# Optimization experiments

Hardware: AMD Instinct MI355X
Metric: run time of the kernel (lower is better)

## Reference

```python
import jax, jax.numpy as jnp
import numpy as np

D_MODEL = 1024
N_HEADS = 16
MAX_LAG = 512
D_K = D_MODEL // N_HEADS


def setup_inputs() -> dict:
    key = jax.random.key(0)
    ks = jax.random.split(key, 11)
    B, S = 2, 2048
    x = jax.random.normal(ks[0], (B, S, D_MODEL), dtype=jnp.float32)
    lag = jax.random.randint(ks[1], (S,), 0, MAX_LAG + 1, dtype=jnp.int64)
    scale = 1.0 / np.sqrt(D_MODEL)
    wq = jax.random.normal(ks[2], (D_MODEL, D_MODEL), dtype=jnp.float32) * scale
    bq = jnp.zeros((D_MODEL,), dtype=jnp.float32)
    wk = jax.random.normal(ks[3], (D_MODEL, D_MODEL), dtype=jnp.float32) * scale
    bk = jnp.zeros((D_MODEL,), dtype=jnp.float32)
    wv = jax.random.normal(ks[4], (D_MODEL, D_MODEL), dtype=jnp.float32) * scale
    bv = jnp.zeros((D_MODEL,), dtype=jnp.float32)
    wo = jax.random.normal(ks[5], (D_MODEL, D_MODEL), dtype=jnp.float32) * scale
    bo = jnp.zeros((D_MODEL,), dtype=jnp.float32)
    lag_bias = jax.random.normal(ks[6], (N_HEADS, MAX_LAG + 1), dtype=jnp.float32) * 0.02
    return {"x": x, "lag": lag, "wq": wq, "bq": bq, "wk": wk, "bk": bk,
            "wv": wv, "bv": bv, "wo": wo, "bo": bo, "lag_bias": lag_bias}


def reference(x, lag, wq, bq, wk, bk, wv, bv, wo, bo, lag_bias):
    B, S, D = x.shape
    H, dk = N_HEADS, D_K
    # projections: torch Linear is x @ W.T + b; here weights stored as (in, out)
    q = (x @ wq + bq).reshape(B, S, H, dk).transpose(0, 2, 1, 3)  # (B,H,S,dk)
    k = (x @ wk + bk).reshape(B, S, H, dk).transpose(0, 2, 1, 3)
    v = (x @ wv + bv).reshape(B, S, H, dk).transpose(0, 2, 1, 3)
    scores = jnp.einsum('bhqd,bhkd->bhqk', q, k) / jnp.sqrt(jnp.float32(dk))
    ld = jnp.abs(lag[:, None] - lag[None, :]).astype(jnp.int32)  # (S,S)
    bias = lag_bias[:, ld]  # (H,S,S)
    attn = jax.nn.softmax(scores + bias[None], axis=-1)
    out = jnp.einsum('bhqk,bhkd->bhqd', attn, v)
    out = out.transpose(0, 2, 1, 3).reshape(B, S, D)
    return out @ wo + bo
```

## Files before the change

### kernel.cpp

```cpp
#include <hip/hip_runtime.h>

typedef __bf16 bf16;
typedef __bf16 bf16x8 __attribute__((ext_vector_type(8)));
typedef float f32x4 __attribute__((ext_vector_type(4)));

__device__ __forceinline__ f32x4 mfma16(bf16x8 a, bf16x8 b, f32x4 c) {
  return __builtin_amdgcn_mfma_f32_16x16x32_bf16(a, b, c, 0, 0, 0);
}
__device__ __forceinline__ void gload16(const bf16* g, bf16* l) {
  __builtin_amdgcn_global_load_lds((const __attribute__((address_space(1))) unsigned int*)g,
                                   (__attribute__((address_space(3))) unsigned int*)l, 16, 0, 0);
}

__global__ __launch_bounds__(256) void cvt_x_kernel(const float* __restrict__ in,
                                                    bf16* __restrict__ out, int n8) {
  int i = blockIdx.x * 256 + threadIdx.x;
  if (i >= n8) return;
  const float4* p = (const float4*)in + (size_t)i * 2;
  float4 f0 = p[0], f1 = p[1];
  bf16x8 o;
  o[0] = (bf16)f0.x; o[1] = (bf16)f0.y; o[2] = (bf16)f0.z; o[3] = (bf16)f0.w;
  o[4] = (bf16)f1.x; o[5] = (bf16)f1.y; o[6] = (bf16)f1.z; o[7] = (bf16)f1.w;
  *((bf16x8*)out + i) = o;
}

__global__ __launch_bounds__(256) void cvt_wt_kernel(const float* __restrict__ in,
                                                     bf16* __restrict__ out) {
  __shared__ float t[64][68];
  int bx = blockIdx.x & 15;
  int by = blockIdx.x >> 4;
  int tid = threadIdx.x;
  int r = tid >> 2, p = tid & 3;
  const float* src = in + (size_t)(by * 64 + r) * 1024 + bx * 64 + p * 16;
#pragma unroll
  for (int j = 0; j < 16; j += 4)
    *(float4*)&t[r][p * 16 + j] = *(const float4*)(src + j);
  __syncthreads();
  int n = tid >> 2, sp = tid & 3;
  bf16 tmp[16];
#pragma unroll
  for (int j = 0; j < 16; ++j) tmp[j] = (bf16)t[sp * 16 + j][n];
  bf16* dst = out + (size_t)(bx * 64 + n) * 1024 + by * 64 + sp * 16;
  *(bf16x8*)dst = *(bf16x8*)&tmp[0];
  *(bf16x8*)(dst + 8) = *(bf16x8*)&tmp[8];
}

__global__ void cvt_bias_kernel(const float* __restrict__ bq, const float* __restrict__ bk,
                                const float* __restrict__ bv, float* __restrict__ out) {
  int i = blockIdx.x * 256 + threadIdx.x;
  if (i < 1024) out[i] = bq[i];
  else if (i < 2048) out[i] = bk[i - 1024];
  else if (i < 3072) out[i] = bv[i - 2048];
}

template <int OUT_BF16>
__global__ __launch_bounds__(256) void gemm_bt_kernel(
    const bf16* __restrict__ A, const bf16* __restrict__ Bt,
    const float* __restrict__ bias, void* __restrict__ C,
    int M, int N, int K, int scale_cols, float scale_val) {
  __shared__ bf16 As[128][40];
  __shared__ bf16 Bs[128][40];
  int bn = blockIdx.x * 128, bm = blockIdx.y * 128;
  int tid = threadIdx.x;
  int l = tid & 63;
  int w = tid >> 6;
  int wr = w >> 1, wc = w & 1;
  int g = l >> 4, c = l & 15;
  int sr = tid >> 2, sk = (tid & 3) * 8;
  const bf16* Ap = A + (size_t)(bm + sr) * K + sk;
  const bf16* Bp = Bt + (size_t)(bn + sr) * K + sk;
  f32x4 acc[4][4] = {};
  for (int k0 = 0; k0 < K; k0 += 32) {
    bf16x8 a0 = *(const bf16x8*)(Ap + k0);
    bf16x8 a1 = *(const bf16x8*)(Ap + (size_t)64 * K + k0);
    bf16x8 b0 = *(const bf16x8*)(Bp + k0);
    bf16x8 b1 = *(const bf16x8*)(Bp + (size_t)64 * K + k0);
    __syncthreads();
    *(bf16x8*)&As[sr][sk] = a0;
    *(bf16x8*)&As[sr + 64][sk] = a1;
    *(bf16x8*)&Bs[sr][sk] = b0;
    *(bf16x8*)&Bs[sr + 64][sk] = b1;
    __syncthreads();
    bf16x8 af[4], bfr[4];
#pragma unroll
    for (int m = 0; m < 4; ++m) af[m] = *(const bf16x8*)&As[wr * 64 + m * 16 + c][g * 8];
#pragma unroll
    for (int n = 0; n < 4; ++n) bfr[n] = *(const bf16x8*)&Bs[wc * 64 + n * 16 + c][g * 8];
#pragma unroll
    for (int m = 0; m < 4; ++m)
#pragma unroll
      for (int n = 0; n < 4; ++n)
        acc[m][n] = mfma16(af[m], bfr[n], acc[m][n]);
  }
  int rowb = bm + wr * 64;
  int colb = bn + wc * 64;
#pragma unroll
  for (int n = 0; n < 4; ++n) {
    int col = colb + n * 16 + c;
    float bv = bias[col];
    float s = (col < scale_cols) ? scale_val : 1.0f;
#pragma unroll
    for (int m = 0; m < 4; ++m) {
      int row = rowb + m * 16 + g * 4;
#pragma unroll
      for (int j = 0; j < 4; ++j) {
        float v = (acc[m][n][j] + bv) * s;
        if (OUT_BF16)
          ((bf16*)C)[(size_t)(row + j) * N + col] = (bf16)v;
        else
          ((float*)C)[(size_t)(row + j) * N + col] = v;
      }
    }
  }
}

__global__ __launch_bounds__(256) void transpose_v_kernel(const bf16* __restrict__ qkv,
                                                          bf16* __restrict__ vt) {
  __shared__ bf16 t[64][72];
  int blk = blockIdx.x;
  int st = blk & 31;
  int h = (blk >> 5) & 15;
  int b = blk >> 9;
  int tid = threadIdx.x;
  int r = tid >> 2, p = tid & 3;
  const bf16* src = qkv + (size_t)(b * 2048 + st * 64 + r) * 3072 + 2048 + h * 64 + p * 16;
  *(bf16x8*)&t[r][p * 16] = *(const bf16x8*)src;
  *(bf16x8*)&t[r][p * 16 + 8] = *(const bf16x8*)(src + 8);
  __syncthreads();
  int d = tid >> 2, sp = tid & 3;
  bf16 tmp[16];
#pragma unroll
  for (int j = 0; j < 16; ++j) tmp[j] = t[sp * 16 + j][d];
  bf16* dst = vt + (size_t)((b * 16 + h) * 64 + d) * 2048 + st * 64 + sp * 16;
  *(bf16x8*)dst = *(bf16x8*)&tmp[0];
  *(bf16x8*)(dst + 8) = *(bf16x8*)&tmp[8];
}

__global__ __launch_bounds__(256) void attn_kernel(
    const bf16* __restrict__ qkv, const bf16* __restrict__ vt,
    const int* __restrict__ lag, const float* __restrict__ lag_bias,
    bf16* __restrict__ out) {
  __shared__ __align__(16) bf16 KsLin[64 * 64];
  __shared__ __align__(16) bf16 VsLin[64 * 64];
  __shared__ __align__(16) bf16 Ps[4][16][72];
  __shared__ float bias_s[516];
  __shared__ int lag_s[2048];

  int blk = blockIdx.x;
  blk = (blk & 7) * 128 + (blk >> 3);
  int qt = blk & 31;
  int h = (blk >> 5) & 15;
  int b = blk >> 9;
  int tid = threadIdx.x;
  int w = tid >> 6, l = tid & 63, g = l >> 4, c = l & 15;

  for (int i = tid; i < 513; i += 256) bias_s[i] = lag_bias[h * 513 + i] * 1.44269504f;
  for (int i = tid; i < 2048; i += 256) lag_s[i] = lag[i];

  int q0 = qt * 64 + w * 16;
  const bf16* qbase = qkv + (size_t)(b * 2048 + q0) * 3072 + h * 64;
  bf16x8 qf[2];
  qf[0] = *(const bf16x8*)(qbase + (size_t)c * 3072 + g * 8);
  qf[1] = *(const bf16x8*)(qbase + (size_t)c * 3072 + 32 + g * 8);

  int swz = (c & 7) << 3;
  int off0 = (g * 8) ^ swz;
  int off1 = off0 ^ 32;

  int r0 = w * 16 + (l >> 3);
  int colE = ((l & 7) ^ (l >> 3)) << 3;
  const bf16* kbase = qkv + (size_t)(b * 2048) * 3072 + 1024 + h * 64;
  const bf16* vbase = vt + (size_t)(b * 16 + h) * 64 * 2048;
  const bf16* kg0 = kbase + (size_t)r0 * 3072 + colE;
  const bf16* kg1 = kbase + (size_t)(r0 + 8) * 3072 + colE;
  const bf16* vg0 = vbase + (size_t)r0 * 2048 + colE;
  const bf16* vg1 = vbase + (size_t)(r0 + 8) * 2048 + colE;
  bf16* kl0 = KsLin + w * 1024;
  bf16* kl1 = KsLin + w * 1024 + 512;
  bf16* vl0 = VsLin + w * 1024;
  bf16* vl1 = VsLin + w * 1024 + 512;

  __syncthreads();
  int lagq[4];
#pragma unroll
  for (int j = 0; j < 4; ++j) lagq[j] = lag_s[q0 + g * 4 + j];

  f32x4 oacc[4] = {};
  float psum[4] = {0.f, 0.f, 0.f, 0.f};

  for (int kt = 0; kt < 2048; kt += 64) {
    __syncthreads();
    gload16(kg0, kl0);
    gload16(kg1, kl1);
    gload16(vg0, vl0);
    gload16(vg1, vl1);
    kg0 += 64 * 3072; kg1 += 64 * 3072; vg0 += 64; vg1 += 64;
    __syncthreads();

    f32x4 sf[4] = {};
    int lagk[4];
#pragma unroll
    for (int kb = 0; kb < 4; ++kb) {
      int row = kb * 16 + c;
      bf16x8 k0 = *(const bf16x8*)&KsLin[row * 64 + off0];
      bf16x8 k1 = *(const bf16x8*)&KsLin[row * 64 + off1];
      sf[kb] = mfma16(qf[0], k0, sf[kb]);
      sf[kb] = mfma16(qf[1], k1, sf[kb]);
      lagk[kb] = lag_s[kt + kb * 16 + c];
    }
#pragma unroll
    for (int kb = 0; kb < 4; ++kb) {
#pragma unroll
      for (int j = 0; j < 4; ++j) {
        int ld = lagq[j] - lagk[kb];
        ld = ld < 0 ? -ld : ld;
        float p = __builtin_amdgcn_exp2f(sf[kb][j] + bias_s[ld]);
        psum[j] += p;
        Ps[w][g * 4 + j][kb * 16 + c] = (bf16)p;
      }
    }
    asm volatile("s_waitcnt lgkmcnt(0)" ::: "memory");
    bf16x8 pa0 = *(const bf16x8*)&Ps[w][c][g * 8];
    bf16x8 pa1 = *(const bf16x8*)&Ps[w][c][32 + g * 8];
#pragma unroll
    for (int n = 0; n < 4; ++n) {
      int row = n * 16 + c;
      bf16x8 v0 = *(const bf16x8*)&VsLin[row * 64 + off0];
      bf16x8 v1 = *(const bf16x8*)&VsLin[row * 64 + off1];
      oacc[n] = mfma16(pa0, v0, oacc[n]);
      oacc[n] = mfma16(pa1, v1, oacc[n]);
    }
  }

#pragma unroll
  for (int j = 0; j < 4; ++j) {
    float s = psum[j];
    s += __shfl_xor(s, 1);
    s += __shfl_xor(s, 2);
    s += __shfl_xor(s, 4);
    s += __shfl_xor(s, 8);
    float inv = 1.f / s;
    bf16* ob = out + (size_t)(b * 2048 + q0 + g * 4 + j) * 1024 + h * 64;
#pragma unroll
    for (int n = 0; n < 4; ++n)
      ob[n * 16 + c] = (bf16)(oacc[n][j] * inv);
  }
}

extern "C" void kernel_launch(void* const* d_in, const int* in_sizes, int n_in,
                              void* d_out, int out_size, void* d_ws, size_t ws_size,
                              hipStream_t stream) {
  const float* x        = (const float*)d_in[0];
  const int*   lag      = (const int*)d_in[1];
  const float* wq       = (const float*)d_in[2];
  const float* bq       = (const float*)d_in[3];
  const float* wk       = (const float*)d_in[4];
  const float* bk       = (const float*)d_in[5];
  const float* wv       = (const float*)d_in[6];
  const float* bv       = (const float*)d_in[7];
  const float* wo       = (const float*)d_in[8];
  const float* bo       = (const float*)d_in[9];
  const float* lag_bias = (const float*)d_in[10];

  char* ws = (char*)d_ws;
  bf16*  xb    = (bf16*)ws;
  bf16*  wqkvt = (bf16*)(ws + (8u  << 20));
  bf16*  wot   = (bf16*)(ws + (14u << 20));
  float* bqkv  = (float*)(ws + (16u << 20));
  bf16*  qkv   = (bf16*)(ws + (17u << 20));
  bf16*  vtb   = (bf16*)(ws + (41u << 20));
  bf16*  aout  = (bf16*)(ws + (49u << 20));

  cvt_x_kernel<<<2048, 256, 0, stream>>>(x, xb, 524288);
  cvt_wt_kernel<<<256, 256, 0, stream>>>(wq, wqkvt);
  cvt_wt_kernel<<<256, 256, 0, stream>>>(wk, wqkvt + (1u << 20));
  cvt_wt_kernel<<<256, 256, 0, stream>>>(wv, wqkvt + (2u << 20));
  cvt_wt_kernel<<<256, 256, 0, stream>>>(wo, wot);
  cvt_bias_kernel<<<12, 256, 0, stream>>>(bq, bk, bv, bqkv);
  gemm_bt_kernel<1><<<dim3(24, 32), 256, 0, stream>>>(
      xb, wqkvt, bqkv, qkv, 4096, 3072, 1024, 1024, 0.125f * 1.44269504f);
  transpose_v_kernel<<<1024, 256, 0, stream>>>(qkv, vtb);
  attn_kernel<<<1024, 256, 0, stream>>>(qkv, vtb, lag, lag_bias, aout);
  gemm_bt_kernel<0><<<dim3(8, 32), 256, 0, stream>>>(
      aout, wot, bo, (float*)d_out, 4096, 1024, 1024, 0, 1.0f);
}
```

Before: 174.2 us.

## Double-buffer K/V tiles in LDS and read lag/bias straight from global

```diff
diff --git a/kernel.cpp b/kernel.cpp
--- a/kernel.cpp
+++ b/kernel.cpp
@@ -140,11 +140,9 @@
     const bf16* __restrict__ qkv, const bf16* __restrict__ vt,
     const int* __restrict__ lag, const float* __restrict__ lag_bias,
     bf16* __restrict__ out) {
-  __shared__ __align__(16) bf16 KsLin[64 * 64];
-  __shared__ __align__(16) bf16 VsLin[64 * 64];
+  __shared__ __align__(16) bf16 Ks[2][64 * 64];
+  __shared__ __align__(16) bf16 Vs[2][64 * 64];
   __shared__ __align__(16) bf16 Ps[4][16][72];
-  __shared__ float bias_s[516];
-  __shared__ int lag_s[2048];
 
   int blk = blockIdx.x;
   blk = (blk & 7) * 128 + (blk >> 3);
@@ -154,14 +152,16 @@
   int tid = threadIdx.x;
   int w = tid >> 6, l = tid & 63, g = l >> 4, c = l & 15;
 
-  for (int i = tid; i < 513; i += 256) bias_s[i] = lag_bias[h * 513 + i] * 1.44269504f;
-  for (int i = tid; i < 2048; i += 256) lag_s[i] = lag[i];
-
   int q0 = qt * 64 + w * 16;
   const bf16* qbase = qkv + (size_t)(b * 2048 + q0) * 3072 + h * 64;
   bf16x8 qf[2];
   qf[0] = *(const bf16x8*)(qbase + (size_t)c * 3072 + g * 8);
   qf[1] = *(const bf16x8*)(qbase + (size_t)c * 3072 + 32 + g * 8);
+
+  int lagq[4];
+#pragma unroll
+  for (int j = 0; j < 4; ++j) lagq[j] = lag[q0 + g * 4 + j];
+  const float* __restrict__ lbh = lag_bias + h * 513;
 
   int swz = (c & 7) << 3;
   int off0 = (g * 8) ^ swz;
@@ -175,38 +175,41 @@
   const bf16* kg1 = kbase + (size_t)(r0 + 8) * 3072 + colE;
   const bf16* vg0 = vbase + (size_t)r0 * 2048 + colE;
   const bf16* vg1 = vbase + (size_t)(r0 + 8) * 2048 + colE;
-  bf16* kl0 = KsLin + w * 1024;
-  bf16* kl1 = KsLin + w * 1024 + 512;
-  bf16* vl0 = VsLin + w * 1024;
-  bf16* vl1 = VsLin + w * 1024 + 512;
-
+
+  gload16(kg0, &Ks[0][w * 1024]);
+  gload16(kg1, &Ks[0][w * 1024 + 512]);
+  gload16(vg0, &Vs[0][w * 1024]);
+  gload16(vg1, &Vs[0][w * 1024 + 512]);
+  kg0 += 64 * 3072; kg1 += 64 * 3072; vg0 += 64; vg1 += 64;
   __syncthreads();
-  int lagq[4];
-#pragma unroll
-  for (int j = 0; j < 4; ++j) lagq[j] = lag_s[q0 + g * 4 + j];
 
   f32x4 oacc[4] = {};
   float psum[4] = {0.f, 0.f, 0.f, 0.f};
+  int cur = 0;
 
   for (int kt = 0; kt < 2048; kt += 64) {
-    __syncthreads();
-    gload16(kg0, kl0);
-    gload16(kg1, kl1);
-    gload16(vg0, vl0);
-    gload16(vg1, vl1);
-    kg0 += 64 * 3072; kg1 += 64 * 3072; vg0 += 64; vg1 += 64;
-    __syncthreads();
+    if (kt + 64 < 2048) {
+      int nxt = cur ^ 1;
+      gload16(kg0, &Ks[nxt][w * 1024]);
+      gload16(kg1, &Ks[nxt][w * 1024 + 512]);
+      gload16(vg0, &Vs[nxt][w * 1024]);
+      gload16(vg1, &Vs[nxt][w * 1024 + 512]);
+      kg0 += 64 * 3072; kg1 += 64 * 3072; vg0 += 64; vg1 += 64;
+    }
+
+    const bf16* Kb = Ks[cur];
+    const bf16* Vb = Vs[cur];
 
     f32x4 sf[4] = {};
     int lagk[4];
 #pragma unroll
     for (int kb = 0; kb < 4; ++kb) {
       int row = kb * 16 + c;
-      bf16x8 k0 = *(const bf16x8*)&KsLin[row * 64 + off0];
-      bf16x8 k1 = *(const bf16x8*)&KsLin[row * 64 + off1];
+      bf16x8 k0 = *(const bf16x8*)&Kb[row * 64 + off0];
+      bf16x8 k1 = *(const bf16x8*)&Kb[row * 64 + off1];
       sf[kb] = mfma16(qf[0], k0, sf[kb]);
       sf[kb] = mfma16(qf[1], k1, sf[kb]);
-      lagk[kb] = lag_s[kt + kb * 16 + c];
+      lagk[kb] = lag[kt + kb * 16 + c];
     }
 #pragma unroll
     for (int kb = 0; kb < 4; ++kb) {
@@ -214,7 +217,7 @@
       for (int j = 0; j < 4; ++j) {
         int ld = lagq[j] - lagk[kb];
         ld = ld < 0 ? -ld : ld;
-        float p = __builtin_amdgcn_exp2f(sf[kb][j] + bias_s[ld]);
+        float p = __builtin_amdgcn_exp2f(fmaf(lbh[ld], 1.44269504f, sf[kb][j]));
         psum[j] += p;
         Ps[w][g * 4 + j][kb * 16 + c] = (bf16)p;
       }
@@ -225,11 +228,14 @@
 #pragma unroll
     for (int n = 0; n < 4; ++n) {
       int row = n * 16 + c;
-      bf16x8 v0 = *(const bf16x8*)&VsLin[row * 64 + off0];
-      bf16x8 v1 = *(const bf16x8*)&VsLin[row * 64 + off1];
+      bf16x8 v0 = *(const bf16x8*)&Vb[row * 64 + off0];
+      bf16x8 v1 = *(const bf16x8*)&Vb[row * 64 + off1];
       oacc[n] = mfma16(pa0, v0, oacc[n]);
       oacc[n] = mfma16(pa1, v1, oacc[n]);
     }
+
+    __syncthreads();
+    cur ^= 1;
   }
 
 #pragma unroll
```

Measured after the change: 237.7 us. 36.5% more time.

## Double-buffer K/V tiles and process 32 query rows per warp in attention

Applied to the files above, without the earlier changes.

```diff
diff --git a/kernel.cpp b/kernel.cpp
--- a/kernel.cpp
+++ b/kernel.cpp
@@ -140,28 +140,33 @@
     const bf16* __restrict__ qkv, const bf16* __restrict__ vt,
     const int* __restrict__ lag, const float* __restrict__ lag_bias,
     bf16* __restrict__ out) {
-  __shared__ __align__(16) bf16 KsLin[64 * 64];
-  __shared__ __align__(16) bf16 VsLin[64 * 64];
-  __shared__ __align__(16) bf16 Ps[4][16][72];
+  __shared__ __align__(16) bf16 Ks0[64 * 64];
+  __shared__ __align__(16) bf16 Vs0[64 * 64];
+  __shared__ __align__(16) bf16 Ks1[64 * 64];
+  __shared__ __align__(16) bf16 Vs1[64 * 64];
+  __shared__ __align__(16) bf16 Ps[4][32][72];
   __shared__ float bias_s[516];
   __shared__ int lag_s[2048];
 
   int blk = blockIdx.x;
-  blk = (blk & 7) * 128 + (blk >> 3);
-  int qt = blk & 31;
-  int h = (blk >> 5) & 15;
-  int b = blk >> 9;
+  blk = (blk & 7) * 64 + (blk >> 3);
+  int qt = blk & 15;
+  int h = (blk >> 4) & 15;
+  int b = blk >> 8;
   int tid = threadIdx.x;
   int w = tid >> 6, l = tid & 63, g = l >> 4, c = l & 15;
 
   for (int i = tid; i < 513; i += 256) bias_s[i] = lag_bias[h * 513 + i] * 1.44269504f;
   for (int i = tid; i < 2048; i += 256) lag_s[i] = lag[i];
 
-  int q0 = qt * 64 + w * 16;
+  int q0 = qt * 128 + w * 32;
   const bf16* qbase = qkv + (size_t)(b * 2048 + q0) * 3072 + h * 64;
-  bf16x8 qf[2];
-  qf[0] = *(const bf16x8*)(qbase + (size_t)c * 3072 + g * 8);
-  qf[1] = *(const bf16x8*)(qbase + (size_t)c * 3072 + 32 + g * 8);
+  bf16x8 qf[2][2];
+#pragma unroll
+  for (int m = 0; m < 2; ++m)
+#pragma unroll
+    for (int kh = 0; kh < 2; ++kh)
+      qf[m][kh] = *(const bf16x8*)(qbase + (size_t)(m * 16 + c) * 3072 + kh * 32 + g * 8);
 
   int swz = (c & 7) << 3;
   int off0 = (g * 8) ^ swz;
@@ -175,76 +180,92 @@
   const bf16* kg1 = kbase + (size_t)(r0 + 8) * 3072 + colE;
   const bf16* vg0 = vbase + (size_t)r0 * 2048 + colE;
   const bf16* vg1 = vbase + (size_t)(r0 + 8) * 2048 + colE;
-  bf16* kl0 = KsLin + w * 1024;
-  bf16* kl1 = KsLin + w * 1024 + 512;
-  bf16* vl0 = VsLin + w * 1024;
-  bf16* vl1 = VsLin + w * 1024 + 512;
-
+
+#define STAGE(KD, VD)                    \
+  do {                                   \
+    gload16(kg0, KD + w * 1024);         \
+    gload16(kg1, KD + w * 1024 + 512);   \
+    gload16(vg0, VD + w * 1024);         \
+    gload16(vg1, VD + w * 1024 + 512);   \
+    kg0 += 64 * 3072; kg1 += 64 * 3072;  \
+    vg0 += 64; vg1 += 64;                \
+  } while (0)
+
+  STAGE(Ks0, Vs0);
   __syncthreads();
-  int lagq[4];
-#pragma unroll
-  for (int j = 0; j < 4; ++j) lagq[j] = lag_s[q0 + g * 4 + j];
-
-  f32x4 oacc[4] = {};
-  float psum[4] = {0.f, 0.f, 0.f, 0.f};
-
-  for (int kt = 0; kt < 2048; kt += 64) {
+
+  int lagq[2][4];
+#pragma unroll
+  for (int m = 0; m < 2; ++m)
+#pragma unroll
+    for (int j = 0; j < 4; ++j) lagq[m][j] = lag_s[q0 + m * 16 + g * 4 + j];
+
+  f32x4 oacc[2][4] = {};
+  float psum[2][4] = {};
+
+#define TILE(KB, VB, KT)                                                          \
+  do {                                                                            \
+    f32x4 sf[2][4] = {};                                                          \
+    int lagk[4];                                                                  \
+    _Pragma("unroll") for (int kb = 0; kb < 4; ++kb) {                            \
+      int row = kb * 16 + c;                                                      \
+      bf16x8 k0 = *(const bf16x8*)&KB[row * 64 + off0];                           \
+      bf16x8 k1 = *(const bf16x8*)&KB[row * 64 + off1];                           \
+      sf[0][kb] = mfma16(qf[0][0], k0, sf[0][kb]);                                \
+      sf[0][kb] = mfma16(qf[0][1], k1, sf[0][kb]);                                \
+      sf[1][kb] = mfma16(qf[1][0], k0, sf[1][kb]);                                \
+      sf[1][kb] = mfma16(qf[1][1], k1, sf[1][kb]);                                \
+      lagk[kb] = lag_s[(KT) + kb * 16 + c];                                       \
+    }                                                                             \
+    _Pragma("unroll") for (int m = 0; m < 2; ++m)                                 \
+    _Pragma("unroll") for (int kb = 0; kb < 4; ++kb)                              \
+    _Pragma("unroll") for (int j = 0; j < 4; ++j) {                               \
+      int ld = lagq[m][j] - lagk[kb];                                             \
+      ld = ld < 0 ? -ld : ld;                                                     \
+      float p = __builtin_amdgcn_exp2f(sf[m][kb][j] + bias_s[ld]);                \
+      psum[m][j] += p;                                                            \
+      Ps[w][m * 16 + g * 4 + j][kb * 16 + c] = (bf16)p;                           \
+    }                                                                             \
+    asm volatile("s_waitcnt lgkmcnt(0)" ::: "memory");                            \
+    _Pragma("unroll") for (int ph = 0; ph < 2; ++ph) {                            \
+      bf16x8 pa0 = *(const bf16x8*)&Ps[w][c][ph * 32 + g * 8];                    \
+      bf16x8 pa1 = *(const bf16x8*)&Ps[w][16 + c][ph * 32 + g * 8];               \
+      int voff = ph ? off1 : off0;                                                \
+      _Pragma("unroll") for (int n = 0; n < 4; ++n) {                             \
+        bf16x8 vf = *(const bf16x8*)&VB[(n * 16 + c) * 64 + voff];                \
+        oacc[0][n] = mfma16(pa0, vf, oacc[0][n]);                                 \
+        oacc[1][n] = mfma16(pa1, vf, oacc[1][n]);                                 \
+      }                                                                           \
+    }                                                                             \
+  } while (0)
+
+  for (int kt = 0; kt < 2048; kt += 128) {
+    if (kt + 64 < 2048) STAGE(Ks1, Vs1);
+    TILE(Ks0, Vs0, kt);
     __syncthreads();
-    gload16(kg0, kl0);
-    gload16(kg1, kl1);
-    gload16(vg0, vl0);
-    gload16(vg1, vl1);
-    kg0 += 64 * 3072; kg1 += 64 * 3072; vg0 += 64; vg1 += 64;
+    if (kt + 128 < 2048) STAGE(Ks0, Vs0);
+    TILE(Ks1, Vs1, kt + 64);
     __syncthreads();
-
-    f32x4 sf[4] = {};
-    int lagk[4];
-#pragma unroll
-    for (int kb = 0; kb < 4; ++kb) {
-      int row = kb * 16 + c;
-      bf16x8 k0 = *(const bf16x8*)&KsLin[row * 64 + off0];
-      bf16x8 k1 = *(const bf16x8*)&KsLin[row * 64 + off1];
-      sf[kb] = mfma16(qf[0], k0, sf[kb]);
-      sf[kb] = mfma16(qf[1], k1, sf[kb]);
-      lagk[kb] = lag_s[kt + kb * 16 + c];
-    }
-#pragma unroll
-    for (int kb = 0; kb < 4; ++kb) {
-#pragma unroll
-      for (int j = 0; j < 4; ++j) {
-        int ld = lagq[j] - lagk[kb];
-        ld = ld < 0 ? -ld : ld;
-        float p = __builtin_amdgcn_exp2f(sf[kb][j] + bias_s[ld]);
-        psum[j] += p;
-        Ps[w][g * 4 + j][kb * 16 + c] = (bf16)p;
-      }
-    }
-    asm volatile("s_waitcnt lgkmcnt(0)" ::: "memory");
-    bf16x8 pa0 = *(const bf16x8*)&Ps[w][c][g * 8];
-    bf16x8 pa1 = *(const bf16x8*)&Ps[w][c][32 + g * 8];
-#pragma unroll
-    for (int n = 0; n < 4; ++n) {
-      int row = n * 16 + c;
-      bf16x8 v0 = *(const bf16x8*)&VsLin[row * 64 + off0];
-      bf16x8 v1 = *(const bf16x8*)&VsLin[row * 64 + off1];
-      oacc[n] = mfma16(pa0, v0, oacc[n]);
-      oacc[n] = mfma16(pa1, v1, oacc[n]);
+  }
+
+#pragma unroll
+  for (int m = 0; m < 2; ++m) {
+#pragma unroll
+    for (int j = 0; j < 4; ++j) {
+      float s = psum[m][j];
+      s += __shfl_xor(s, 1);
+      s += __shfl_xor(s, 2);
+      s += __shfl_xor(s, 4);
+      s += __shfl_xor(s, 8);
+      float inv = 1.f / s;
+      bf16* ob = out + (size_t)(b * 2048 + q0 + m * 16 + g * 4 + j) * 1024 + h * 64;
+#pragma unroll
+      for (int n = 0; n < 4; ++n)
+        ob[n * 16 + c] = (bf16)(oacc[m][n][j] * inv);
     }
   }
-
-#pragma unroll
-  for (int j = 0; j < 4; ++j) {
-    float s = psum[j];
-    s += __shfl_xor(s, 1);
-    s += __shfl_xor(s, 2);
-    s += __shfl_xor(s, 4);
-    s += __shfl_xor(s, 8);
-    float inv = 1.f / s;
-    bf16* ob = out + (size_t)(b * 2048 + q0 + g * 4 + j) * 1024 + h * 64;
-#pragma unroll
-    for (int n = 0; n < 4; ++n)
-      ob[n * 16 + c] = (bf16)(oacc[n][j] * inv);
-  }
+#undef STAGE
+#undef TILE
 }
 
 extern "C" void kernel_launch(void* const* d_in, const int* in_sizes, int n_in,
@@ -280,7 +301,7 @@
   gemm_bt_kernel<1><<<dim3(24, 32), 256, 0, stream>>>(
       xb, wqkvt, bqkv, qkv, 4096, 3072, 1024, 1024, 0.125f * 1.44269504f);
   transpose_v_kernel<<<1024, 256, 0, stream>>>(qkv, vtb);
-  attn_kernel<<<1024, 256, 0, stream>>>(qkv, vtb, lag, lag_bias, aout);
+  attn_kernel<<<512, 256, 0, stream>>>(qkv, vtb, lag, lag_bias, aout);
   gemm_bt_kernel<0><<<dim3(8, 32), 256, 0, stream>>>(
       aout, wot, bo, (float*)d_out, 4096, 1024, 1024, 0, 1.0f);
 }
```

New measurement: 171.0 us. Within noise of the previous version (-1.8%).
